# Kernel tuning notes

Measured on AMD Instinct MI355X. Metric: run time of the kernel, lower is better.

The kernel has to match this reference:

```python
import jax, jax.numpy as jnp
import numpy as np

N = 100_000      # nodes
E = 1_600_000    # directed edges (avg degree 16)
F_IN = 128       # num_node_features
H = 8            # heads in conv1
C = 32           # hidden_channels
G = 64           # graphs in batch
NC = 10          # num_classes


def setup_inputs() -> dict:
    key = jax.random.key(0)
    ks = jax.random.split(key, 12)
    gl = lambda k, shape, fan: (jax.random.normal(k, shape, jnp.float32) / np.sqrt(fan)).astype(jnp.float32)
    return {
        "x": jax.random.normal(ks[0], (N, F_IN), jnp.float32),
        "edge_index": jax.random.randint(ks[1], (2, E), 0, N, dtype=jnp.int32),
        "batch": jnp.sort(jax.random.randint(ks[2], (N,), 0, G, dtype=jnp.int32)),
        "W1": gl(ks[3], (F_IN, H * C), F_IN),
        "att_src1": gl(ks[4], (H, C), C),
        "att_dst1": gl(ks[5], (H, C), C),
        "b1": jnp.zeros((H * C,), jnp.float32),
        "W2": gl(ks[6], (H * C, C), H * C),
        "att_src2": gl(ks[7], (1, C), C),
        "att_dst2": gl(ks[8], (1, C), C),
        "b2": jnp.zeros((C,), jnp.float32),
        "Wlin": gl(ks[9], (C, NC), C),
        "blin": jnp.zeros((NC,), jnp.float32),
    }


def gat_conv(x, src, dst, W, att_src, att_dst, bias, heads, ch, concat):
    """PyG GATConv (eval mode): gather, LeakyReLU(0.2) scores, segment softmax over dst, scatter-sum."""
    n = x.shape[0]
    h = (x @ W).reshape(n, heads, ch)                     # [N,H,C]
    a_s = jnp.sum(h * att_src, axis=-1)                   # [N,H]
    a_d = jnp.sum(h * att_dst, axis=-1)                   # [N,H]
    e = jax.nn.leaky_relu(a_s[src] + a_d[dst], 0.2)       # [E,H]
    m = jax.ops.segment_max(e, dst, num_segments=n)       # [N,H], stable softmax
    p = jnp.exp(e - m[dst])
    z = jax.ops.segment_sum(p, dst, num_segments=n)
    coef = p / (z[dst] + 1e-16)                           # [E,H]
    out = jax.ops.segment_sum(coef[:, :, None] * h[src], dst, num_segments=n)  # [N,H,C]
    out = out.reshape(n, heads * ch) if concat else out.mean(axis=1)
    return out + bias


def reference(x, edge_index, batch, W1, att_src1, att_dst1, b1,
              W2, att_src2, att_dst2, b2, Wlin, blin):
    n = x.shape[0]
    loops = jnp.arange(n, dtype=edge_index.dtype)         # GATConv add_self_loops=True
    src = jnp.concatenate([edge_index[0], loops])
    dst = jnp.concatenate([edge_index[1], loops])

    h = gat_conv(x, src, dst, W1, att_src1, att_dst1, b1, H, C, concat=True)
    h = jax.nn.elu(h)                                     # dropout is identity in eval
    h = gat_conv(h, src, dst, W2, att_src2, att_dst2, b2, 1, C, concat=False)

    # global_mean_pool over graph ids
    sums = jax.ops.segment_sum(h, batch, num_segments=G)  # [G,C]
    cnts = jax.ops.segment_sum(jnp.ones((n,), h.dtype), batch, num_segments=G)
    pooled = sums / jnp.maximum(cnts, 1.0)[:, None]

    return pooled @ Wlin + blin                           # [G,NC]
```

## Files before the change

### kernel.cpp

```cpp
#include <hip/hip_runtime.h>
#include <cstdint>

#define NN 100000
#define EE 1600000
#define GG 64
#define FIN 128
#define HC 256
#define NC 10

typedef short v8s __attribute__((ext_vector_type(8)));
typedef float v4f __attribute__((ext_vector_type(4)));

static __device__ __forceinline__ float lrelu(float x) { return x > 0.f ? x : 0.2f * x; }
static __device__ __forceinline__ float bf2f(unsigned short b) {
  return __uint_as_float(((unsigned int)b) << 16);
}
static __device__ __forceinline__ unsigned short f2bf(float f) {
  unsigned int u = __float_as_uint(f);
  unsigned int r = (u + 0x7FFFu + ((u >> 16) & 1u)) >> 16;
  return (unsigned short)r;
}
static __device__ __forceinline__ unsigned int pk2bf(float a, float b) {
  return (unsigned int)f2bf(a) | ((unsigned int)f2bf(b) << 16);
}
static __device__ __forceinline__ void unpack2(unsigned int u, float& f0, float& f1) {
  f0 = __uint_as_float(u << 16);
  f1 = __uint_as_float(u & 0xFFFF0000u);
}

__global__ __launch_bounds__(256) void k_prepx(const float* __restrict__ x,
                                               unsigned short* __restrict__ xb,
                                               unsigned int* __restrict__ counts) {
  const int idx = blockIdx.x * 256 + threadIdx.x;
  const int i4 = idx * 4;
  float4 v = *(const float4*)(x + i4);
  ushort4 u;
  u.x = f2bf(v.x); u.y = f2bf(v.y); u.z = f2bf(v.z); u.w = f2bf(v.w);
  *(ushort4*)(xb + i4) = u;
  if (idx < NN) counts[idx] = 0u;
}

__global__ void k_prep(const float* __restrict__ W1, unsigned short* __restrict__ W1tg) {
  const int b = blockIdx.x, t = threadIdx.x;
  if (t < 128) W1tg[b * 128 + t] = f2bf(W1[t * HC + b]);
}

__global__ __launch_bounds__(256) void k_gemm1(const unsigned short* __restrict__ xb,
                                               const unsigned short* __restrict__ W1tg,
                                               const float* __restrict__ att_src1,
                                               const float* __restrict__ att_dst1,
                                               unsigned short* __restrict__ h1b,
                                               float* __restrict__ as1,
                                               float* __restrict__ ad1) {
  const int t = threadIdx.x;
  const int m0 = blockIdx.x * 64;
  const int n0 = blockIdx.y * 128;
  const int hb = blockIdx.y * 4;
  const int lane = t & 63;
  const int wm = t >> 6;
  const int ml = lane & 15;
  const int quad = lane >> 4;
  int row = m0 + wm * 16 + ml; if (row >= NN) row = NN - 1;
  v4f acc[8];
#pragma unroll
  for (int tt = 0; tt < 8; ++tt) acc[tt] = (v4f){0.f, 0.f, 0.f, 0.f};
#pragma unroll
  for (int kk = 0; kk < 4; ++kk) {
    const int k0 = kk * 32 + quad * 8;
    v8s a = *(const v8s*)(xb + (size_t)row * FIN + k0);
#pragma unroll
    for (int tt = 0; tt < 8; ++tt) {
      v8s b = *(const v8s*)(W1tg + (size_t)(n0 + tt * 16 + ml) * FIN + k0);
      acc[tt] = __builtin_amdgcn_mfma_f32_16x16x32_bf16(a, b, acc[tt], 0, 0, 0);
    }
  }
#pragma unroll
  for (int tt = 0; tt < 8; ++tt) {
#pragma unroll
    for (int r = 0; r < 4; ++r) {
      int rg = m0 + wm * 16 + quad * 4 + r;
      if (rg < NN) h1b[(size_t)rg * HC + n0 + tt * 16 + ml] = f2bf(acc[tt][r]);
    }
  }
  float ps[4][4], pd[4][4];
#pragma unroll
  for (int i = 0; i < 4; ++i)
#pragma unroll
    for (int r = 0; r < 4; ++r) { ps[i][r] = 0.f; pd[i][r] = 0.f; }
#pragma unroll
  for (int i = 0; i < 4; ++i) {
#pragma unroll
    for (int half = 0; half < 2; ++half) {
      const int tt = 2 * i + half;
      const float a_s = att_src1[(hb + i) * 32 + half * 16 + ml];
      const float a_d = att_dst1[(hb + i) * 32 + half * 16 + ml];
#pragma unroll
      for (int r = 0; r < 4; ++r) {
        ps[i][r] += acc[tt][r] * a_s;
        pd[i][r] += acc[tt][r] * a_d;
      }
    }
  }
#pragma unroll
  for (int i = 0; i < 4; ++i) {
#pragma unroll
    for (int r = 0; r < 4; ++r) {
      float s = ps[i][r], d = pd[i][r];
      s += __shfl_xor(s, 1, 64); s += __shfl_xor(s, 2, 64);
      s += __shfl_xor(s, 4, 64); s += __shfl_xor(s, 8, 64);
      d += __shfl_xor(d, 1, 64); d += __shfl_xor(d, 2, 64);
      d += __shfl_xor(d, 4, 64); d += __shfl_xor(d, 8, 64);
      ps[i][r] = s; pd[i][r] = d;
    }
  }
  if (ml == 0) {
#pragma unroll
    for (int r = 0; r < 4; ++r) {
      int rg = m0 + wm * 16 + quad * 4 + r;
      if (rg < NN) {
#pragma unroll
        for (int i = 0; i < 4; ++i) {
          as1[rg * 8 + hb + i] = ps[i][r];
          ad1[rg * 8 + hb + i] = pd[i][r];
        }
      }
    }
  }
}

__global__ void k_count(const int* __restrict__ ei, int* __restrict__ counts) {
  int e = blockIdx.x * 256 + threadIdx.x;
  if (e < EE) atomicAdd(&counts[ei[EE + e]], 1);
}

__global__ void k_scan1(const int* __restrict__ counts, int* __restrict__ offs,
                        int* __restrict__ bsums) {
  __shared__ int s[256];
  const int t = threadIdx.x;
  const int i = blockIdx.x * 256 + t;
  int v = (i < NN) ? counts[i] : 0;
  s[t] = v;
  __syncthreads();
  for (int off = 1; off < 256; off <<= 1) {
    int tv = (t >= off) ? s[t - off] : 0;
    __syncthreads();
    s[t] += tv;
    __syncthreads();
  }
  if (i < NN) offs[i] = s[t] - v;
  if (t == 255) bsums[blockIdx.x] = s[255];
}

__global__ void k_scan2(int* __restrict__ bsums, int nb) {
  __shared__ int s[512];
  const int t = threadIdx.x;
  int v = (t < nb) ? bsums[t] : 0;
  s[t] = v;
  __syncthreads();
  for (int off = 1; off < 512; off <<= 1) {
    int tv = (t >= off) ? s[t - off] : 0;
    __syncthreads();
    s[t] += tv;
    __syncthreads();
  }
  if (t < nb) bsums[t] = s[t] - v;
}

__global__ void k_scan3(int* __restrict__ offs, const int* __restrict__ bsums,
                        int* __restrict__ cursor) {
  const int i = blockIdx.x * 256 + threadIdx.x;
  if (i < NN) {
    int v = offs[i] + bsums[i >> 8];
    offs[i] = v;
    cursor[i] = v;
  }
  if (i == 0) offs[NN] = EE;
}

__global__ void k_scatter(const int* __restrict__ ei, int* __restrict__ cursor,
                          const float* __restrict__ as1, const float* __restrict__ ad1,
                          int* __restrict__ esrc, uint4* __restrict__ wt16) {
  int e = blockIdx.x * 256 + threadIdx.x;
  if (e < EE) {
    int s = ei[e];
    int d = ei[EE + e];
    int p = atomicAdd(&cursor[d], 1);
    esrc[p] = s;
    float4 a0 = *(const float4*)(as1 + s * 8);
    float4 a1 = *(const float4*)(as1 + s * 8 + 4);
    float4 b0 = *(const float4*)(ad1 + d * 8);
    float4 b1 = *(const float4*)(ad1 + d * 8 + 4);
    uint4 u;
    u.x = pk2bf(__expf(lrelu(a0.x + b0.x)), __expf(lrelu(a0.y + b0.y)));
    u.y = pk2bf(__expf(lrelu(a0.z + b0.z)), __expf(lrelu(a0.w + b0.w)));
    u.z = pk2bf(__expf(lrelu(a1.x + b1.x)), __expf(lrelu(a1.y + b1.y)));
    u.w = pk2bf(__expf(lrelu(a1.z + b1.z)), __expf(lrelu(a1.w + b1.w)));
    wt16[p] = u;
  }
}

__global__ __launch_bounds__(128) void k_agg1(const unsigned short* __restrict__ h1b,
                                              const float* __restrict__ as1,
                                              const float* __restrict__ ad1,
                                              const int* __restrict__ offs,
                                              const int* __restrict__ esrc,
                                              const unsigned int* __restrict__ wt4,
                                              const float* __restrict__ b1,
                                              const float* __restrict__ W2,
                                              const float* __restrict__ att_src2,
                                              const float* __restrict__ att_dst2,
                                              unsigned short* __restrict__ h2b,
                                              float* __restrict__ as2,
                                              float* __restrict__ ad2) {
  __shared__ float wl[2][32][8];
  __shared__ float sv[256];
  __shared__ float zsh[2][8];
  __shared__ float sp[4][33];
  const int t = threadIdx.x;
  const int lane = t & 63;
  const int w = t >> 6;
  const int head = lane >> 3;
  const int n0 = blockIdx.x * 2;
  const int o0 = offs[n0], o1 = offs[n0 + 1], o2 = offs[n0 + 2];
  const uint2* h1u2 = (const uint2*)h1b;

  int sreg[2] = {0, 0};
  const int cnt0 = min(32, o1 - o0);
  const int cnt1 = min(32, o2 - o1);
  if (lane < cnt0) sreg[0] = esrc[o0 + lane];
  if (lane < cnt1) sreg[1] = esrc[o1 + lane];
  {
    const int j = t >> 2, hq = t & 3;
    if (j < cnt0) {
      float f0, f1; unpack2(wt4[(size_t)(o0 + j) * 4 + hq], f0, f1);
      *(float2*)&wl[0][j][hq * 2] = make_float2(f0, f1);
    }
    if (j < cnt1) {
      float f0, f1; unpack2(wt4[(size_t)(o1 + j) * 4 + hq], f0, f1);
      *(float2*)&wl[1][j][hq * 2] = make_float2(f0, f1);
    }
  }
  __syncthreads();

  for (int ns = 0; ns < 2; ++ns) {
    const int n = n0 + ns;
    const int sBeg = ns ? o1 : o0;
    const int sEnd = ns ? o2 : o1;
    float acc0 = 0.f, acc1 = 0.f, acc2 = 0.f, acc3 = 0.f, z = 0.f;
    if (w == 0) {
      float w0 = __expf(lrelu(as1[n * 8 + head] + ad1[n * 8 + head]));
      z = w0;
      uint2 q = h1u2[(size_t)n * 64 + lane];
      float f0, f1, f2, f3; unpack2(q.x, f0, f1); unpack2(q.y, f2, f3);
      acc0 = w0 * f0; acc1 = w0 * f1; acc2 = w0 * f2; acc3 = w0 * f3;
    }
    int sregc = sreg[ns];
    for (int base = sBeg; base < sEnd; base += 32) {
      const int cnt = min(32, sEnd - base);
      if (base != sBeg) {
        sregc = 0;
        if (lane < cnt) sregc = esrc[base + lane];
        __syncthreads();
        const int j = t >> 2, hq = t & 3;
        if (j < cnt) {
          float f0, f1; unpack2(wt4[(size_t)(base + j) * 4 + hq], f0, f1);
          *(float2*)&wl[ns][j][hq * 2] = make_float2(f0, f1);
        }
        __syncthreads();
      }
#pragma unroll 8
      for (int j2 = w; j2 < cnt; j2 += 2) {
        int sj = __builtin_amdgcn_readlane(sregc, j2);
        uint2 q = h1u2[(size_t)sj * 64 + lane];
        float wv = wl[ns][j2][head];
        float f0, f1, f2, f3; unpack2(q.x, f0, f1); unpack2(q.y, f2, f3);
        z += wv;
        acc0 += wv * f0; acc1 += wv * f1; acc2 += wv * f2; acc3 += wv * f3;
      }
    }

    __syncthreads();
    if (w == 0) {
      *(float4*)&sv[4 * lane] = make_float4(acc0, acc1, acc2, acc3);
      if ((lane & 7) == 0) zsh[0][head] = z;
    }
    __syncthreads();
    if (w == 1) {
      float4 p = *(float4*)&sv[4 * lane];
      p.x += acc0; p.y += acc1; p.z += acc2; p.w += acc3;
      *(float4*)&sv[4 * lane] = p;
      if ((lane & 7) == 0) zsh[1][head] = z;
    }
    __syncthreads();
    {
      const int ho = t >> 4;
      const float zf = zsh[0][ho] + zsh[1][ho];
      const float zi = 1.0f / (zf + 1e-16f);
      float2 bb = *(const float2*)(b1 + 2 * t);
      float v0 = sv[2 * t] * zi + bb.x;
      float v1 = sv[2 * t + 1] * zi + bb.y;
      v0 = v0 > 0.f ? v0 : (__expf(v0) - 1.0f);
      v1 = v1 > 0.f ? v1 : (__expf(v1) - 1.0f);
      __syncthreads();
      sv[2 * t] = v0; sv[2 * t + 1] = v1;
    }
    __syncthreads();
    const int c = t & 31, rr = t >> 5;
    const float* svp = sv + rr * 64;
    const float* w2p = W2 + rr * 64 * 32 + c;
    float p = 0.f;
#pragma unroll 16
    for (int kk = 0; kk < 64; ++kk) p += svp[kk] * w2p[kk * 32];
    sp[rr][c] = p;
    __syncthreads();
    if (t < 32) {
      float hv = sp[0][t] + sp[1][t] + sp[2][t] + sp[3][t];
      h2b[(size_t)n * 32 + t] = f2bf(hv);
      float ps = hv * att_src2[t];
      float pd = hv * att_dst2[t];
#pragma unroll
      for (int m = 16; m >= 1; m >>= 1) {
        ps += __shfl_xor(ps, m, 64);
        pd += __shfl_xor(pd, m, 64);
      }
      if (t == 0) { as2[n] = ps; ad2[n] = pd; }
    }
    __syncthreads();
  }
}

__global__ __launch_bounds__(256) void k_agg2(const unsigned short* __restrict__ h2b,
                                              const float* __restrict__ as2,
                                              const float* __restrict__ ad2,
                                              const int* __restrict__ offs,
                                              const int* __restrict__ esrc,
                                              const float* __restrict__ b2,
                                              float* __restrict__ h3) {
  const int t = threadIdx.x;
  const int lane = t & 63;
  const int wv = t >> 6;
  const int n = blockIdx.x * 4 + wv;
  const int col = lane & 15;
  const int slot = lane >> 4;
  const unsigned int* h2u = (const unsigned int*)h2b;
  const int start = offs[n], end = offs[n + 1];
  const float adn = ad2[n];
  float z = 0.f, acc0 = 0.f, acc1 = 0.f;
  if (slot == 0) {
    float w0 = __expf(lrelu(as2[n] + adn));
    unsigned int q = h2u[(size_t)n * 16 + col];
    float f0, f1; unpack2(q, f0, f1);
    z = w0; acc0 = w0 * f0; acc1 = w0 * f1;
  }
  for (int base = start; base < end; base += 64) {
    const int cnt = min(64, end - base);
    int sreg = 0; float wreg = 0.f;
    if (lane < cnt) {
      sreg = esrc[base + lane];
      wreg = __expf(lrelu(as2[sreg] + adn));
    }
    const int jmax = (cnt + 3) >> 2;
#pragma unroll 4
    for (int j = 0; j < jmax; ++j) {
      const int e = 4 * j + slot;
      int sj = __shfl(sreg, e, 64);
      float wj = __shfl(wreg, e, 64);
      if (e < cnt) {
        unsigned int q = h2u[(size_t)sj * 16 + col];
        float f0, f1; unpack2(q, f0, f1);
        z += wj; acc0 += wj * f0; acc1 += wj * f1;
      }
    }
  }
  acc0 += __shfl_xor(acc0, 16, 64); acc0 += __shfl_xor(acc0, 32, 64);
  acc1 += __shfl_xor(acc1, 16, 64); acc1 += __shfl_xor(acc1, 32, 64);
  z    += __shfl_xor(z, 16, 64);    z    += __shfl_xor(z, 32, 64);
  if (slot == 0) {
    const float zi = 1.0f / (z + 1e-16f);
    float2 bb = *(const float2*)(b2 + 2 * col);
    float2 o;
    o.x = acc0 * zi + bb.x;
    o.y = acc1 * zi + bb.y;
    *(float2*)(h3 + (size_t)n * 32 + 2 * col) = o;
  }
}

__global__ __launch_bounds__(256) void k_poolfin(const float* __restrict__ h3,
                                                 const int* __restrict__ batch,
                                                 const float* __restrict__ Wlin,
                                                 const float* __restrict__ blin,
                                                 float* __restrict__ out) {
  __shared__ int bounds[2];
  __shared__ float red[8][33];
  __shared__ float mean[32];
  const int g = blockIdx.x;
  const int t = threadIdx.x;
  if (t < 2) {
    int target = g + t;
    int lo = 0, hi = NN;
    while (lo < hi) { int mid = (lo + hi) >> 1; if (batch[mid] < target) lo = mid + 1; else hi = mid; }
    bounds[t] = lo;
  }
  __syncthreads();
  const int lo = bounds[0], hi = bounds[1];
  const int rr = t >> 5, c = t & 31;
  float a = 0.f;
  for (int r = lo + rr; r < hi; r += 8) a += h3[(size_t)r * 32 + c];
  red[rr][c] = a;
  __syncthreads();
  if (rr == 0) {
    float s = 0.f;
#pragma unroll
    for (int i = 0; i < 8; ++i) s += red[i][c];
    float ct = (float)(hi - lo);
    ct = ct > 1.f ? ct : 1.f;
    mean[c] = s / ct;
  }
  __syncthreads();
  if (t < NC) {
    float acc = 0.f;
#pragma unroll
    for (int cc = 0; cc < 32; ++cc) acc += mean[cc] * Wlin[cc * NC + t];
    out[g * NC + t] = acc + blin[t];
  }
}

extern "C" void kernel_launch(void* const* d_in, const int* in_sizes, int n_in,
                              void* d_out, int out_size, void* d_ws, size_t ws_size,
                              hipStream_t stream) {
  const float* x        = (const float*)d_in[0];
  const int*   ei       = (const int*)d_in[1];
  const int*   batch    = (const int*)d_in[2];
  const float* W1       = (const float*)d_in[3];
  const float* att_src1 = (const float*)d_in[4];
  const float* att_dst1 = (const float*)d_in[5];
  const float* b1       = (const float*)d_in[6];
  const float* W2       = (const float*)d_in[7];
  const float* att_src2 = (const float*)d_in[8];
  const float* att_dst2 = (const float*)d_in[9];
  const float* b2       = (const float*)d_in[10];
  const float* Wlin     = (const float*)d_in[11];
  const float* blin     = (const float*)d_in[12];
  float* out = (float*)d_out;
  char* ws = (char*)d_ws;

  unsigned short* h1b  = (unsigned short*)(ws + 0);
  unsigned short* xb   = (unsigned short*)(ws + 51200000);
  float* as1    = (float*)(ws + 76800000);
  float* ad1    = (float*)(ws + 80000000);
  int* counts   = (int*)(ws + 83200000);
  int* offs     = (int*)(ws + 83600000);
  int* cursor   = (int*)(ws + 84000256);
  int* esrc     = (int*)(ws + 84400256);
  int* bsums    = (int*)(ws + 90800256);
  unsigned short* h2b = (unsigned short*)(ws + 90802048);
  float* as2    = (float*)(ws + 97202048);
  float* ad2    = (float*)(ws + 97602048);
  unsigned short* W1tg = (unsigned short*)(ws + 98002048);
  uint4* wt16   = (uint4*)(ws + 98067584);
  float* h3     = (float*)(ws + 98067584);

  const int nb_scan = (NN + 255) / 256;

  k_prepx<<<12500, 256, 0, stream>>>(x, xb, (unsigned int*)counts);
  k_prep<<<256, 128, 0, stream>>>(W1, W1tg);

  dim3 g1((NN + 63) / 64, 2);
  k_gemm1<<<g1, 256, 0, stream>>>(xb, W1tg, att_src1, att_dst1, h1b, as1, ad1);

  k_count<<<(EE + 255) / 256, 256, 0, stream>>>(ei, counts);
  k_scan1<<<nb_scan, 256, 0, stream>>>(counts, offs, bsums);
  k_scan2<<<1, 512, 0, stream>>>(bsums, nb_scan);
  k_scan3<<<nb_scan, 256, 0, stream>>>(offs, bsums, cursor);
  k_scatter<<<(EE + 255) / 256, 256, 0, stream>>>(ei, cursor, as1, ad1, esrc, wt16);

  k_agg1<<<NN / 2, 128, 0, stream>>>(h1b, as1, ad1, offs, esrc, (const unsigned int*)wt16,
                                     b1, W2, att_src2, att_dst2, h2b, as2, ad2);

  k_agg2<<<NN / 4, 256, 0, stream>>>(h2b, as2, ad2, offs, esrc, b2, h3);
  k_poolfin<<<GG, 256, 0, stream>>>(h3, batch, Wlin, blin, out);
}
```

Baseline: 670.9 us.

## Compute edge weights in agg1, one wave per node, MFMA W2 projection

The scatter kernel no longer computes and stores per-edge bf16 attention weights. The layer-1 aggregation now recomputes exp(lrelu(a_s+a_d)) inline per edge, which removes a 16-byte-per-edge write and read round trip. The aggregation kernel is restructured so each wave handles one node with no cross-wave reduction or block syncs in the edge loop. The per-node 256x32 W2 projection for four nodes is done with bf16 MFMA using a hi/lo split of both operands to keep near-fp32 accuracy. This adds a small W2 prep kernel and an extra gather of as1 per edge, plus exp work per head-lane.

New measurement: 670.0 us. Within noise of the previous version (-0.1%).

```diff
diff --git a/kernel.cpp b/kernel.cpp
--- a/kernel.cpp
+++ b/kernel.cpp
@@ -19,9 +19,6 @@
   unsigned int u = __float_as_uint(f);
   unsigned int r = (u + 0x7FFFu + ((u >> 16) & 1u)) >> 16;
   return (unsigned short)r;
-}
-static __device__ __forceinline__ unsigned int pk2bf(float a, float b) {
-  return (unsigned int)f2bf(a) | ((unsigned int)f2bf(b) << 16);
 }
 static __device__ __forceinline__ void unpack2(unsigned int u, float& f0, float& f1) {
   f0 = __uint_as_float(u << 16);
@@ -45,6 +42,17 @@
   if (t < 128) W1tg[b * 128 + t] = f2bf(W1[t * HC + b]);
 }
 
+__global__ void k_prepw2(const float* __restrict__ W2,
+                         unsigned short* __restrict__ W2thi,
+                         unsigned short* __restrict__ W2tlo) {
+  const int b = blockIdx.x;
+  const int t = threadIdx.x;
+  float w = W2[t * 32 + b];
+  unsigned short hi = f2bf(w);
+  W2thi[b * 256 + t] = hi;
+  W2tlo[b * 256 + t] = f2bf(w - bf2f(hi));
+}
+
 __global__ __launch_bounds__(256) void k_gemm1(const unsigned short* __restrict__ xb,
                                                const unsigned short* __restrict__ W1tg,
                                                const float* __restrict__ att_src1,
@@ -178,154 +186,123 @@
 }
 
 __global__ void k_scatter(const int* __restrict__ ei, int* __restrict__ cursor,
-                          const float* __restrict__ as1, const float* __restrict__ ad1,
-                          int* __restrict__ esrc, uint4* __restrict__ wt16) {
+                          int* __restrict__ esrc) {
   int e = blockIdx.x * 256 + threadIdx.x;
   if (e < EE) {
     int s = ei[e];
     int d = ei[EE + e];
     int p = atomicAdd(&cursor[d], 1);
     esrc[p] = s;
-    float4 a0 = *(const float4*)(as1 + s * 8);
-    float4 a1 = *(const float4*)(as1 + s * 8 + 4);
-    float4 b0 = *(const float4*)(ad1 + d * 8);
-    float4 b1 = *(const float4*)(ad1 + d * 8 + 4);
-    uint4 u;
-    u.x = pk2bf(__expf(lrelu(a0.x + b0.x)), __expf(lrelu(a0.y + b0.y)));
-    u.y = pk2bf(__expf(lrelu(a0.z + b0.z)), __expf(lrelu(a0.w + b0.w)));
-    u.z = pk2bf(__expf(lrelu(a1.x + b1.x)), __expf(lrelu(a1.y + b1.y)));
-    u.w = pk2bf(__expf(lrelu(a1.z + b1.z)), __expf(lrelu(a1.w + b1.w)));
-    wt16[p] = u;
-  }
-}
-
-__global__ __launch_bounds__(128) void k_agg1(const unsigned short* __restrict__ h1b,
+  }
+}
+
+__global__ __launch_bounds__(256) void k_agg1(const unsigned short* __restrict__ h1b,
                                               const float* __restrict__ as1,
                                               const float* __restrict__ ad1,
                                               const int* __restrict__ offs,
                                               const int* __restrict__ esrc,
-                                              const unsigned int* __restrict__ wt4,
                                               const float* __restrict__ b1,
-                                              const float* __restrict__ W2,
+                                              const unsigned short* __restrict__ W2thi,
+                                              const unsigned short* __restrict__ W2tlo,
                                               const float* __restrict__ att_src2,
                                               const float* __restrict__ att_dst2,
                                               unsigned short* __restrict__ h2b,
                                               float* __restrict__ as2,
                                               float* __restrict__ ad2) {
-  __shared__ float wl[2][32][8];
-  __shared__ float sv[256];
-  __shared__ float zsh[2][8];
-  __shared__ float sp[4][33];
+  __shared__ __attribute__((aligned(16))) unsigned short o1hi[4][256];
+  __shared__ __attribute__((aligned(16))) unsigned short o1lo[4][256];
   const int t = threadIdx.x;
   const int lane = t & 63;
   const int w = t >> 6;
+  const int n0 = blockIdx.x * 4;
+  const int n = n0 + w;
   const int head = lane >> 3;
-  const int n0 = blockIdx.x * 2;
-  const int o0 = offs[n0], o1 = offs[n0 + 1], o2 = offs[n0 + 2];
-  const uint2* h1u2 = (const uint2*)h1b;
-
-  int sreg[2] = {0, 0};
-  const int cnt0 = min(32, o1 - o0);
-  const int cnt1 = min(32, o2 - o1);
-  if (lane < cnt0) sreg[0] = esrc[o0 + lane];
-  if (lane < cnt1) sreg[1] = esrc[o1 + lane];
+  const uint2* __restrict__ h1u2 = (const uint2*)h1b;
+  const int start = offs[n], end = offs[n + 1];
+  const float adn = ad1[n * 8 + head];
+
+  float z, a0, a1, a2, a3;
   {
-    const int j = t >> 2, hq = t & 3;
-    if (j < cnt0) {
-      float f0, f1; unpack2(wt4[(size_t)(o0 + j) * 4 + hq], f0, f1);
-      *(float2*)&wl[0][j][hq * 2] = make_float2(f0, f1);
-    }
-    if (j < cnt1) {
-      float f0, f1; unpack2(wt4[(size_t)(o1 + j) * 4 + hq], f0, f1);
-      *(float2*)&wl[1][j][hq * 2] = make_float2(f0, f1);
-    }
-  }
-  __syncthreads();
-
-  for (int ns = 0; ns < 2; ++ns) {
-    const int n = n0 + ns;
-    const int sBeg = ns ? o1 : o0;
-    const int sEnd = ns ? o2 : o1;
-    float acc0 = 0.f, acc1 = 0.f, acc2 = 0.f, acc3 = 0.f, z = 0.f;
-    if (w == 0) {
-      float w0 = __expf(lrelu(as1[n * 8 + head] + ad1[n * 8 + head]));
-      z = w0;
-      uint2 q = h1u2[(size_t)n * 64 + lane];
+    float w0 = __expf(lrelu(as1[n * 8 + head] + adn));
+    uint2 q = h1u2[(size_t)n * 64 + lane];
+    float f0, f1, f2, f3; unpack2(q.x, f0, f1); unpack2(q.y, f2, f3);
+    z = w0; a0 = w0 * f0; a1 = w0 * f1; a2 = w0 * f2; a3 = w0 * f3;
+  }
+  for (int base = start; base < end; base += 64) {
+    const int cnt = min(64, end - base);
+    int sreg = 0;
+    if (lane < cnt) sreg = esrc[base + lane];
+#pragma unroll 8
+    for (int j = 0; j < cnt; ++j) {
+      const int sj = __builtin_amdgcn_readlane(sreg, j);
+      const float sc = as1[sj * 8 + head];
+      const uint2 q = h1u2[(size_t)sj * 64 + lane];
+      const float wv = __expf(lrelu(sc + adn));
       float f0, f1, f2, f3; unpack2(q.x, f0, f1); unpack2(q.y, f2, f3);
-      acc0 = w0 * f0; acc1 = w0 * f1; acc2 = w0 * f2; acc3 = w0 * f3;
-    }
-    int sregc = sreg[ns];
-    for (int base = sBeg; base < sEnd; base += 32) {
-      const int cnt = min(32, sEnd - base);
-      if (base != sBeg) {
-        sregc = 0;
-        if (lane < cnt) sregc = esrc[base + lane];
-        __syncthreads();
-        const int j = t >> 2, hq = t & 3;
-        if (j < cnt) {
-          float f0, f1; unpack2(wt4[(size_t)(base + j) * 4 + hq], f0, f1);
-          *(float2*)&wl[ns][j][hq * 2] = make_float2(f0, f1);
-        }
-        __syncthreads();
+      z += wv;
+      a0 += wv * f0; a1 += wv * f1; a2 += wv * f2; a3 += wv * f3;
+    }
+  }
+  {
+    const float zi = 1.0f / (z + 1e-16f);
+    const float4 bb = *(const float4*)(b1 + 4 * lane);
+    float v0 = a0 * zi + bb.x;
+    float v1 = a1 * zi + bb.y;
+    float v2 = a2 * zi + bb.z;
+    float v3 = a3 * zi + bb.w;
+    v0 = v0 > 0.f ? v0 : (__expf(v0) - 1.0f);
+    v1 = v1 > 0.f ? v1 : (__expf(v1) - 1.0f);
+    v2 = v2 > 0.f ? v2 : (__expf(v2) - 1.0f);
+    v3 = v3 > 0.f ? v3 : (__expf(v3) - 1.0f);
+    ushort4 hh, ll;
+    hh.x = f2bf(v0); hh.y = f2bf(v1); hh.z = f2bf(v2); hh.w = f2bf(v3);
+    ll.x = f2bf(v0 - bf2f(hh.x));
+    ll.y = f2bf(v1 - bf2f(hh.y));
+    ll.z = f2bf(v2 - bf2f(hh.z));
+    ll.w = f2bf(v3 - bf2f(hh.w));
+    *(ushort4*)&o1hi[w][4 * lane] = hh;
+    *(ushort4*)&o1lo[w][4 * lane] = ll;
+  }
+  __syncthreads();
+  if (w == 0) {
+    const int ml = lane & 15;
+    const int quad = lane >> 4;
+    const int mr = ml & 3;
+    v4f acc[2];
+    acc[0] = (v4f){0.f, 0.f, 0.f, 0.f};
+    acc[1] = (v4f){0.f, 0.f, 0.f, 0.f};
+#pragma unroll
+    for (int kk = 0; kk < 8; ++kk) {
+      const int k0 = kk * 32 + quad * 8;
+      v8s ah = *(const v8s*)&o1hi[mr][k0];
+      v8s al = *(const v8s*)&o1lo[mr][k0];
+#pragma unroll
+      for (int tt = 0; tt < 2; ++tt) {
+        v8s bh = *(const v8s*)(W2thi + (size_t)(tt * 16 + ml) * 256 + k0);
+        v8s bl = *(const v8s*)(W2tlo + (size_t)(tt * 16 + ml) * 256 + k0);
+        acc[tt] = __builtin_amdgcn_mfma_f32_16x16x32_bf16(ah, bh, acc[tt], 0, 0, 0);
+        acc[tt] = __builtin_amdgcn_mfma_f32_16x16x32_bf16(al, bh, acc[tt], 0, 0, 0);
+        acc[tt] = __builtin_amdgcn_mfma_f32_16x16x32_bf16(ah, bl, acc[tt], 0, 0, 0);
       }
-#pragma unroll 8
-      for (int j2 = w; j2 < cnt; j2 += 2) {
-        int sj = __builtin_amdgcn_readlane(sregc, j2);
-        uint2 q = h1u2[(size_t)sj * 64 + lane];
-        float wv = wl[ns][j2][head];
-        float f0, f1, f2, f3; unpack2(q.x, f0, f1); unpack2(q.y, f2, f3);
-        z += wv;
-        acc0 += wv * f0; acc1 += wv * f1; acc2 += wv * f2; acc3 += wv * f3;
+    }
+    if (quad == 0) {
+      const float s0 = att_src2[ml], s1 = att_src2[16 + ml];
+      const float d0 = att_dst2[ml], d1 = att_dst2[16 + ml];
+#pragma unroll
+      for (int r = 0; r < 4; ++r) {
+        const int nn = n0 + r;
+        const float h0 = acc[0][r], h1v = acc[1][r];
+        h2b[(size_t)nn * 32 + ml] = f2bf(h0);
+        h2b[(size_t)nn * 32 + 16 + ml] = f2bf(h1v);
+        float ps = h0 * s0 + h1v * s1;
+        float pd = h0 * d0 + h1v * d1;
+        ps += __shfl_xor(ps, 1, 64); ps += __shfl_xor(ps, 2, 64);
+        ps += __shfl_xor(ps, 4, 64); ps += __shfl_xor(ps, 8, 64);
+        pd += __shfl_xor(pd, 1, 64); pd += __shfl_xor(pd, 2, 64);
+        pd += __shfl_xor(pd, 4, 64); pd += __shfl_xor(pd, 8, 64);
+        if (ml == 0) { as2[nn] = ps; ad2[nn] = pd; }
       }
     }
-
-    __syncthreads();
-    if (w == 0) {
-      *(float4*)&sv[4 * lane] = make_float4(acc0, acc1, acc2, acc3);
-      if ((lane & 7) == 0) zsh[0][head] = z;
-    }
-    __syncthreads();
-    if (w == 1) {
-      float4 p = *(float4*)&sv[4 * lane];
-      p.x += acc0; p.y += acc1; p.z += acc2; p.w += acc3;
-      *(float4*)&sv[4 * lane] = p;
-      if ((lane & 7) == 0) zsh[1][head] = z;
-    }
-    __syncthreads();
-    {
-      const int ho = t >> 4;
-      const float zf = zsh[0][ho] + zsh[1][ho];
-      const float zi = 1.0f / (zf + 1e-16f);
-      float2 bb = *(const float2*)(b1 + 2 * t);
-      float v0 = sv[2 * t] * zi + bb.x;
-      float v1 = sv[2 * t + 1] * zi + bb.y;
-      v0 = v0 > 0.f ? v0 : (__expf(v0) - 1.0f);
-      v1 = v1 > 0.f ? v1 : (__expf(v1) - 1.0f);
-      __syncthreads();
-      sv[2 * t] = v0; sv[2 * t + 1] = v1;
-    }
-    __syncthreads();
-    const int c = t & 31, rr = t >> 5;
-    const float* svp = sv + rr * 64;
-    const float* w2p = W2 + rr * 64 * 32 + c;
-    float p = 0.f;
-#pragma unroll 16
-    for (int kk = 0; kk < 64; ++kk) p += svp[kk] * w2p[kk * 32];
-    sp[rr][c] = p;
-    __syncthreads();
-    if (t < 32) {
-      float hv = sp[0][t] + sp[1][t] + sp[2][t] + sp[3][t];
-      h2b[(size_t)n * 32 + t] = f2bf(hv);
-      float ps = hv * att_src2[t];
-      float pd = hv * att_dst2[t];
-#pragma unroll
-      for (int m = 16; m >= 1; m >>= 1) {
-        ps += __shfl_xor(ps, m, 64);
-        pd += __shfl_xor(pd, m, 64);
-      }
-      if (t == 0) { as2[n] = ps; ad2[n] = pd; }
-    }
-    __syncthreads();
   }
 }
 
@@ -444,8 +421,9 @@
   float* out = (float*)d_out;
   char* ws = (char*)d_ws;
 
-  unsigned short* h1b  = (unsigned short*)(ws + 0);
-  unsigned short* xb   = (unsigned short*)(ws + 51200000);
+  unsigned short* h1b   = (unsigned short*)(ws + 0);
+  unsigned short* xb    = (unsigned short*)(ws + 51200000);
+  float* h3     = (float*)(ws + 51200000);
   float* as1    = (float*)(ws + 76800000);
   float* ad1    = (float*)(ws + 80000000);
   int* counts   = (int*)(ws + 83200000);
@@ -453,17 +431,18 @@
   int* cursor   = (int*)(ws + 84000256);
   int* esrc     = (int*)(ws + 84400256);
   int* bsums    = (int*)(ws + 90800256);
-  unsigned short* h2b = (unsigned short*)(ws + 90802048);
-  float* as2    = (float*)(ws + 97202048);
-  float* ad2    = (float*)(ws + 97602048);
-  unsigned short* W1tg = (unsigned short*)(ws + 98002048);
-  uint4* wt16   = (uint4*)(ws + 98067584);
-  float* h3     = (float*)(ws + 98067584);
+  unsigned short* h2b   = (unsigned short*)(ws + 90802304);
+  float* as2    = (float*)(ws + 97202304);
+  float* ad2    = (float*)(ws + 97602304);
+  unsigned short* W1tg  = (unsigned short*)(ws + 98002304);
+  unsigned short* W2thi = (unsigned short*)(ws + 98067840);
+  unsigned short* W2tlo = (unsigned short*)(ws + 98084224);
 
   const int nb_scan = (NN + 255) / 256;
 
   k_prepx<<<12500, 256, 0, stream>>>(x, xb, (unsigned int*)counts);
   k_prep<<<256, 128, 0, stream>>>(W1, W1tg);
+  k_prepw2<<<32, 256, 0, stream>>>(W2, W2thi, W2tlo);
 
   dim3 g1((NN + 63) / 64, 2);
   k_gemm1<<<g1, 256, 0, stream>>>(xb, W1tg, att_src1, att_dst1, h1b, as1, ad1);
@@ -472,10 +451,10 @@
   k_scan1<<<nb_scan, 256, 0, stream>>>(counts, offs, bsums);
   k_scan2<<<1, 512, 0, stream>>>(bsums, nb_scan);
   k_scan3<<<nb_scan, 256, 0, stream>>>(offs, bsums, cursor);
-  k_scatter<<<(EE + 255) / 256, 256, 0, stream>>>(ei, cursor, as1, ad1, esrc, wt16);
-
-  k_agg1<<<NN / 2, 128, 0, stream>>>(h1b, as1, ad1, offs, esrc, (const unsigned int*)wt16,
-                                     b1, W2, att_src2, att_dst2, h2b, as2, ad2);
+  k_scatter<<<(EE + 255) / 256, 256, 0, stream>>>(ei, cursor, esrc);
+
+  k_agg1<<<NN / 4, 256, 0, stream>>>(h1b, as1, ad1, offs, esrc, b1, W2thi, W2tlo,
+                                     att_src2, att_dst2, h2b, as2, ad2);
 
   k_agg2<<<NN / 4, 256, 0, stream>>>(h2b, as2, ad2, offs, esrc, b2, h3);
   k_poolfin<<<GG, 256, 0, stream>>>(h3, batch, Wlin, blin, out);
```
